# Kernel tuning notes

Hardware: AMD Instinct MI355X
Metric: run time of the kernel (lower is better)

## Reference

```python
import jax, jax.numpy as jnp
import numpy as np

B, D, K, C = 32, 128, 512, 10  # batch, input dim, inner dim, clusters (all hardcoded in source)


def setup_inputs() -> dict:
    key = jax.random.key(0)
    k1, k2, k3, k4 = jax.random.split(key, 4)
    x_batch = jax.random.normal(k1, (B, D), dtype=jnp.float32)
    mu_c = jax.random.normal(k2, (C, D), dtype=jnp.float32)
    # parameters: torch.rand -> uniform [0,1)
    U = jax.random.uniform(k3, (D, K), dtype=jnp.float32)
    V = jax.random.uniform(k4, (D, K), dtype=jnp.float32)
    return {"x_batch": x_batch, "mu_c": mu_c, "U": U, "V": V}


def reference(x_batch, mu_c, U, V):
    # Original loops over batch: h_i = (mu_c @ V) @ (x_i @ U), then log_softmax over
    # the length-10 vector (dim=0 per sample). Batched equivalent:
    fac1 = x_batch @ U          # [B, K]
    fac2 = mu_c @ V             # [C, K]
    h = fac1 @ fac2.T           # [B, C]
    return jax.nn.log_softmax(h, axis=-1)
```

## Files before the change

kernel.cpp:

```cpp
#include <hip/hip_runtime.h>
#include <hip/hip_bf16.h>
#include <math.h>

#define BB 32
#define DD 128
#define KK 512
#define CC 10
#define KSPLIT 4
#define KCH (KK / KSPLIT)

__global__ __launch_bounds__(KCH) void fac_kernel(
    const float* __restrict__ x, const float* __restrict__ mu,
    const float* __restrict__ U, const float* __restrict__ V,
    float* __restrict__ fac)
{
    const int r  = blockIdx.x;
    const int ks = blockIdx.y;
    const int k  = ks * KCH + threadIdx.x;

    const float* __restrict__ row = (r < BB) ? (x + r * DD) : (mu + (r - BB) * DD);
    const float* __restrict__ W   = (r < BB) ? U : V;

    float acc0 = 0.0f, acc1 = 0.0f;
    #pragma unroll 16
    for (int d = 0; d < DD; d += 2) {
        acc0 = fmaf(row[d],     W[d * KK + k],       acc0);
        acc1 = fmaf(row[d + 1], W[(d + 1) * KK + k], acc1);
    }
    fac[r * KK + k] = acc0 + acc1;
}

__global__ __launch_bounds__(64) void h_softmax_kernel(
    const float* __restrict__ fac, float* __restrict__ out)
{
    const int b    = blockIdx.x;
    const int lane = threadIdx.x;

    const float* __restrict__ f1 = fac + b * KK;
    const float* __restrict__ f2 = fac + BB * KK;

    const float4* f1v = (const float4*)(f1 + lane * 8);
    const float4 p0 = f1v[0];
    const float4 p1 = f1v[1];

    float hrow[CC];
    #pragma unroll
    for (int c = 0; c < CC; ++c) {
        const float4* f2v = (const float4*)(f2 + c * KK + lane * 8);
        const float4 q0 = f2v[0];
        const float4 q1 = f2v[1];
        float s = p0.x * q0.x + p0.y * q0.y + p0.z * q0.z + p0.w * q0.w
                + p1.x * q1.x + p1.y * q1.y + p1.z * q1.z + p1.w * q1.w;
        #pragma unroll
        for (int off = 32; off > 0; off >>= 1)
            s += __shfl_xor(s, off);
        hrow[c] = s;
    }

    float mx = hrow[0];
    #pragma unroll
    for (int c = 1; c < CC; ++c) mx = fmaxf(mx, hrow[c]);
    float sum = 0.0f;
    #pragma unroll
    for (int c = 0; c < CC; ++c) sum += __expf(hrow[c] - mx);
    const float lse = mx + __logf(sum);

    if (lane < CC) {
        float v = hrow[0];
        #pragma unroll
        for (int c = 1; c < CC; ++c) v = (lane == c) ? hrow[c] : v;
        out[b * CC + lane] = v - lse;
    }
}

extern "C" void kernel_launch(void* const* d_in, const int* in_sizes, int n_in,
                              void* d_out, int out_size, void* d_ws, size_t ws_size,
                              hipStream_t stream)
{
    const float* x  = (const float*)d_in[0];
    const float* mu = (const float*)d_in[1];
    const float* U  = (const float*)d_in[2];
    const float* V  = (const float*)d_in[3];
    float* out = (float*)d_out;
    float* fac = (float*)d_ws;

    dim3 gridA(BB + CC, KSPLIT);
    fac_kernel<<<gridA, KCH, 0, stream>>>(x, mu, U, V, fac);
    h_softmax_kernel<<<BB, 64, 0, stream>>>(fac, out);
}
```

Baseline: 63.83 us.

## Fuse factor and softmax kernels using a global atomic counter barrier

Merges the two kernel launches into a single kernel. Every block computes its factor slice, then increments a global counter. The first-chunk block of each batch row spins until all blocks have finished before computing the dot products and the log-softmax. This removes the second launch and the inter-kernel gap, but adds a memset launch and a spin-wait that relies on all 168 blocks being co-resident.

```diff
diff --git a/kernel.cpp b/kernel.cpp
--- a/kernel.cpp
+++ b/kernel.cpp
@@ -8,15 +8,19 @@
 #define CC 10
 #define KSPLIT 4
 #define KCH (KK / KSPLIT)
+#define NBLK ((BB + CC) * KSPLIT)
 
-__global__ __launch_bounds__(KCH) void fac_kernel(
+__global__ __launch_bounds__(KCH) void fused_kernel(
     const float* __restrict__ x, const float* __restrict__ mu,
     const float* __restrict__ U, const float* __restrict__ V,
-    float* __restrict__ fac)
+    unsigned int* __restrict__ counter,
+    float* __restrict__ fac,
+    float* __restrict__ out)
 {
-    const int r  = blockIdx.x;
-    const int ks = blockIdx.y;
-    const int k  = ks * KCH + threadIdx.x;
+    const int blk = blockIdx.x;
+    const int r   = blk / KSPLIT;
+    const int ks  = blk - r * KSPLIT;
+    const int k   = ks * KCH + threadIdx.x;
 
     const float* __restrict__ row = (r < BB) ? (x + r * DD) : (mu + (r - BB) * DD);
     const float* __restrict__ W   = (r < BB) ? U : V;
@@ -28,48 +32,55 @@
         acc1 = fmaf(row[d + 1], W[(d + 1) * KK + k], acc1);
     }
     fac[r * KK + k] = acc0 + acc1;
-}
 
-__global__ __launch_bounds__(64) void h_softmax_kernel(
-    const float* __restrict__ fac, float* __restrict__ out)
-{
-    const int b    = blockIdx.x;
-    const int lane = threadIdx.x;
+    __threadfence();
+    __syncthreads();
+    if (threadIdx.x == 0) atomicAdd(counter, 1u);
 
-    const float* __restrict__ f1 = fac + b * KK;
-    const float* __restrict__ f2 = fac + BB * KK;
+    if (r < BB && ks == 0) {
+        while (__hip_atomic_load(counter, __ATOMIC_ACQUIRE,
+                                 __HIP_MEMORY_SCOPE_AGENT) < NBLK) {
+            __builtin_amdgcn_s_sleep(1);
+        }
 
-    const float4* f1v = (const float4*)(f1 + lane * 8);
-    const float4 p0 = f1v[0];
-    const float4 p1 = f1v[1];
+        if (threadIdx.x < 64) {
+            const int lane = threadIdx.x;
+            const float* __restrict__ f1 = fac + r * KK;
+            const float* __restrict__ f2 = fac + BB * KK;
 
-    float hrow[CC];
-    #pragma unroll
-    for (int c = 0; c < CC; ++c) {
-        const float4* f2v = (const float4*)(f2 + c * KK + lane * 8);
-        const float4 q0 = f2v[0];
-        const float4 q1 = f2v[1];
-        float s = p0.x * q0.x + p0.y * q0.y + p0.z * q0.z + p0.w * q0.w
-                + p1.x * q1.x + p1.y * q1.y + p1.z * q1.z + p1.w * q1.w;
-        #pragma unroll
-        for (int off = 32; off > 0; off >>= 1)
-            s += __shfl_xor(s, off);
-        hrow[c] = s;
-    }
+            const float4* f1v = (const float4*)(f1 + lane * 8);
+            const float4 p0 = f1v[0];
+            const float4 p1 = f1v[1];
 
-    float mx = hrow[0];
-    #pragma unroll
-    for (int c = 1; c < CC; ++c) mx = fmaxf(mx, hrow[c]);
-    float sum = 0.0f;
-    #pragma unroll
-    for (int c = 0; c < CC; ++c) sum += __expf(hrow[c] - mx);
-    const float lse = mx + __logf(sum);
+            float hrow[CC];
+            #pragma unroll
+            for (int c = 0; c < CC; ++c) {
+                const float4* f2v = (const float4*)(f2 + c * KK + lane * 8);
+                const float4 q0 = f2v[0];
+                const float4 q1 = f2v[1];
+                float s = p0.x * q0.x + p0.y * q0.y + p0.z * q0.z + p0.w * q0.w
+                        + p1.x * q1.x + p1.y * q1.y + p1.z * q1.z + p1.w * q1.w;
+                #pragma unroll
+                for (int off = 32; off > 0; off >>= 1)
+                    s += __shfl_xor(s, off);
+                hrow[c] = s;
+            }
 
-    if (lane < CC) {
-        float v = hrow[0];
-        #pragma unroll
-        for (int c = 1; c < CC; ++c) v = (lane == c) ? hrow[c] : v;
-        out[b * CC + lane] = v - lse;
+            float mx = hrow[0];
+            #pragma unroll
+            for (int c = 1; c < CC; ++c) mx = fmaxf(mx, hrow[c]);
+            float sum = 0.0f;
+            #pragma unroll
+            for (int c = 0; c < CC; ++c) sum += __expf(hrow[c] - mx);
+            const float lse = mx + __logf(sum);
+
+            if (lane < CC) {
+                float v = hrow[0];
+                #pragma unroll
+                for (int c = 1; c < CC; ++c) v = (lane == c) ? hrow[c] : v;
+                out[r * CC + lane] = v - lse;
+            }
+        }
     }
 }
 
@@ -82,9 +93,10 @@
     const float* U  = (const float*)d_in[2];
     const float* V  = (const float*)d_in[3];
     float* out = (float*)d_out;
-    float* fac = (float*)d_ws;
 
-    dim3 gridA(BB + CC, KSPLIT);
-    fac_kernel<<<gridA, KCH, 0, stream>>>(x, mu, U, V, fac);
-    h_softmax_kernel<<<BB, 64, 0, stream>>>(fac, out);
+    unsigned int* counter = (unsigned int*)d_ws;
+    float* fac = (float*)((char*)d_ws + 512);
+
+    hipMemsetAsync(counter, 0, sizeof(unsigned int), stream);
+    fused_kernel<<<NBLK, KCH, 0, stream>>>(x, mu, U, V, counter, fac, out);
 }
```

Result: slower. 74.84 us (+17.2%).
